# Kernel tuning notes

Hardware: AMD Instinct MI355X
Metric: run time of the kernel (lower is better)

The kernel has to match this reference:

```python
import jax, jax.numpy as jnp
import numpy as np
import math

EMBED_DIM = 512
NUM_CLASSES = 100000
BATCH = 512
MARGIN = 0.5
SCALE = 64.0
EASY_MARGIN = False
COS_M = math.cos(MARGIN)
SIN_M = math.sin(MARGIN)
TH = math.cos(math.pi - MARGIN)
MM = math.sin(math.pi - MARGIN) * MARGIN


def setup_inputs() -> dict:
    key = jax.random.key(0)
    k1, k2, k3 = jax.random.split(key, 3)
    inp = jax.random.normal(k1, (BATCH, EMBED_DIM), dtype=jnp.float32)
    # xavier-uniform init for weight [num_classes, embedding_dim]
    limit = math.sqrt(6.0 / (NUM_CLASSES + EMBED_DIM))
    weight = jax.random.uniform(k2, (NUM_CLASSES, EMBED_DIM), dtype=jnp.float32,
                                minval=-limit, maxval=limit)
    target = jax.random.randint(k3, (BATCH,), 0, NUM_CLASSES, dtype=jnp.int64)
    return {"input": inp, "weight": weight, "target": target}


def _l2_normalize(x, axis, eps=1e-12):
    # matches F.normalize(p=2): x / max(||x||, eps)
    n = jnp.sqrt(jnp.sum(x * x, axis=axis, keepdims=True))
    return x / jnp.maximum(n, eps)


def reference(input, weight, target):
    x = _l2_normalize(input, axis=1)                      # [B, D]
    w = _l2_normalize(weight, axis=1)                     # [C, D]
    cosine = jnp.einsum('bd,cd->bc', x, w)                # [B, C]
    # margin only affects the target logit; compute it per-row (same math as
    # the full-matrix where + one_hot blend in the original).
    cos_t = jnp.take_along_axis(cosine, target[:, None].astype(jnp.int32), axis=1)[:, 0]  # [B]
    sin_t = jnp.sqrt(jnp.clip(1.0 - cos_t * cos_t, 0.0, None))
    phi_t = cos_t * COS_M - sin_t * SIN_M
    if EASY_MARGIN:
        phi_t = jnp.where(cos_t > 0, phi_t, cos_t)
    else:
        phi_t = jnp.where(cos_t > TH, phi_t, cos_t - MM)
    # cross-entropy with scaled logits: logsumexp over modified logits - target logit
    # modified logits differ from `cosine*SCALE` only at the target column.
    rows = jnp.arange(cosine.shape[0])
    logits = cosine.at[rows, target.astype(jnp.int32)].set(phi_t) * SCALE  # [B, C]
    lse = jax.scipy.special.logsumexp(logits, axis=1)     # [B]
    loss = jnp.mean(lse - SCALE * phi_t)
    return loss
```

## Files before the change

### kernel.cpp

```cpp
#include <hip/hip_runtime.h>
#include <math.h>


#define NB 512
#define ND 512
#define NC 100000
#define BK 32
#define NCHUNK 16
#define CT 64
#define NTILE 1563
#define REP 64
#define FSCALE 64.0f
#define C_COS_M 0.8775825618903728f
#define C_SIN_M 0.479425538604203f
#define C_TH  (-0.8775825618903728f)
#define C_MM  0.2397127693021015f

#define SWZA(b) ((b) ^ (((b) >> 3) & 48))
#define SWZW(b) ((b) ^ (((b) >> 3) & 112))

typedef __bf16 bf16x8 __attribute__((ext_vector_type(8)));
typedef __bf16 bf16x4 __attribute__((ext_vector_type(4)));
typedef float  f32x4  __attribute__((ext_vector_type(4)));
typedef __attribute__((address_space(1))) unsigned int GU;
typedef __attribute__((address_space(3))) unsigned int LU;

__global__ void pack_x_kernel(const float* __restrict__ x, __bf16* __restrict__ xp) {
  const int b = blockIdx.x;
  const int t = threadIdx.x;
  float4 v = reinterpret_cast<const float4*>(x + (size_t)b * ND)[t];
  float ss = v.x*v.x + v.y*v.y + v.z*v.z + v.w*v.w;
  #pragma unroll
  for (int m = 1; m < 64; m <<= 1) ss += __shfl_xor(ss, m);
  __shared__ float sred[2];
  if ((t & 63) == 0) sred[t >> 6] = ss;
  __syncthreads();
  const float rn = rsqrtf(fmaxf(sred[0] + sred[1], 1e-24f));
  bf16x4 o;
  o[0] = (__bf16)(v.x * rn); o[1] = (__bf16)(v.y * rn);
  o[2] = (__bf16)(v.z * rn); o[3] = (__bf16)(v.w * rn);
  const int k = 4 * t;
  const int chunk = k >> 5;
  const int lb = b * 64 + (k & 31) * 2;
  char* dst = (char*)xp + (size_t)chunk * (NB * BK * 2) + SWZA(lb);
  *reinterpret_cast<bf16x4*>(dst) = o;
}

__global__ void prep_w_kernel(const float* __restrict__ w, __bf16* __restrict__ wp) {
  const int row  = blockIdx.x * 4 + (threadIdx.x >> 6);
  const int lane = threadIdx.x & 63;
  if (row >= NTILE * CT) return;
  const int srow = min(row, NC - 1);
  const float4* src = reinterpret_cast<const float4*>(w + (size_t)srow * ND);
  float4 v0 = src[lane * 2];
  float4 v1 = src[lane * 2 + 1];
  float ss = v0.x*v0.x + v0.y*v0.y + v0.z*v0.z + v0.w*v0.w
           + v1.x*v1.x + v1.y*v1.y + v1.z*v1.z + v1.w*v1.w;
  #pragma unroll
  for (int m = 1; m < 64; m <<= 1) ss += __shfl_xor(ss, m);
  float rn = rsqrtf(fmaxf(ss, 1e-24f));
  if (row >= NC) rn = 0.f;
  const int tile = row >> 6;
  const int r64  = row & 63;
  char* base = (char*)wp + (size_t)tile * (NCHUNK * 4096);
  #pragma unroll
  for (int j = 0; j < 2; ++j) {
    const float4 v = j ? v1 : v0;
    bf16x4 o;
    o[0] = (__bf16)(v.x * rn); o[1] = (__bf16)(v.y * rn);
    o[2] = (__bf16)(v.z * rn); o[3] = (__bf16)(v.w * rn);
    const int k  = lane * 8 + j * 4;
    const int lb = r64 * 64 + (k & 31) * 2;
    *reinterpret_cast<bf16x4*>(base + (k >> 5) * 4096 + SWZA(lb)) = o;
  }
}

__global__ void cosphi_kernel(const float* __restrict__ x, const float* __restrict__ w,
                              const int* __restrict__ tgt,
                              float* __restrict__ cos_t, float* __restrict__ phi_t) {
  const int b = blockIdx.x;
  const int lane = threadIdx.x;
  const int t = tgt[b];
  const float4* xr = reinterpret_cast<const float4*>(x + (size_t)b * ND);
  const float4* wr = reinterpret_cast<const float4*>(w + (size_t)t * ND);
  float dp = 0.f, xs = 0.f, ws = 0.f;
  #pragma unroll
  for (int j = 0; j < 2; ++j) {
    float4 xv = xr[lane * 2 + j];
    float4 wv = wr[lane * 2 + j];
    dp += xv.x*wv.x + xv.y*wv.y + xv.z*wv.z + xv.w*wv.w;
    xs += xv.x*xv.x + xv.y*xv.y + xv.z*xv.z + xv.w*xv.w;
    ws += wv.x*wv.x + wv.y*wv.y + wv.z*wv.z + wv.w*wv.w;
  }
  #pragma unroll
  for (int m = 1; m < 64; m <<= 1) {
    dp += __shfl_xor(dp, m);
    xs += __shfl_xor(xs, m);
    ws += __shfl_xor(ws, m);
  }
  if (lane == 0) {
    float c = dp * rsqrtf(fmaxf(xs, 1e-24f)) * rsqrtf(fmaxf(ws, 1e-24f));
    c = fminf(fmaxf(c, -1.f), 1.f);
    float s = sqrtf(fmaxf(1.f - c * c, 0.f));
    float phi = c * C_COS_M - s * C_SIN_M;
    phi = (c > C_TH) ? phi : (c - C_MM);
    cos_t[b] = c;
    phi_t[b] = phi;
  }
}

__global__ __launch_bounds__(512, 4) void gemm_lse_kernel(
    const __bf16* __restrict__ xp, const __bf16* __restrict__ wp,
    float* __restrict__ gsum) {
  __shared__ __align__(16) char As[2 * NB * BK * 2];
  __shared__ __align__(16) char Ws[2 * CT * BK * 2];

  const int tid  = threadIdx.x;
  const int wv   = tid >> 6;
  const int lane = tid & 63;
  const int bc   = blockIdx.x * CT;

  const char* ag = (const char*)xp + wv * 1024 + lane * 16;
  const char* wg = (const char*)wp + (size_t)blockIdx.x * (NCHUNK * 4096)
                   + wv * 1024 + lane * 16;

  {
    char* la = As + wv * 1024;
    #pragma unroll
    for (int j = 0; j < 4; ++j)
      __builtin_amdgcn_global_load_lds((const GU*)(ag + j * 8192),
                                       (LU*)(la + j * 8192), 16, 0, 0);
    if (wv < 4)
      __builtin_amdgcn_global_load_lds((const GU*)wg, (LU*)(Ws + wv * 1024),
                                       16, 0, 0);
  }

  const int m_w  = wv * 64;
  const int ra   = lane & 15;
  const int quad = lane >> 4;
  int aoff[4], boff[4];
  #pragma unroll
  for (int rt = 0; rt < 4; ++rt)
    aoff[rt] = SWZA((m_w + rt * 16 + ra) * 64 + quad * 16);
  #pragma unroll
  for (int ct = 0; ct < 4; ++ct)
    boff[ct] = SWZA((ct * 16 + ra) * 64 + quad * 16);

  f32x4 acc[4][4] = {};

  __syncthreads();

  for (int c = 0; c < NCHUNK; ++c) {
    const int cur = c & 1;
    if (c + 1 < NCHUNK) {
      const char* a1 = ag + (size_t)(c + 1) * (NB * BK * 2);
      char* la = As + (cur ^ 1) * (NB * BK * 2) + wv * 1024;
      #pragma unroll
      for (int j = 0; j < 4; ++j)
        __builtin_amdgcn_global_load_lds((const GU*)(a1 + j * 8192),
                                         (LU*)(la + j * 8192), 16, 0, 0);
      if (wv < 4)
        __builtin_amdgcn_global_load_lds((const GU*)(wg + (size_t)(c + 1) * 4096),
                                         (LU*)(Ws + (cur ^ 1) * 4096 + wv * 1024),
                                         16, 0, 0);
    }

    const char* asb = As + cur * (NB * BK * 2);
    const char* wsb = Ws + cur * 4096;
    bf16x8 af[4], bfr[4];
    #pragma unroll
    for (int rt = 0; rt < 4; ++rt)
      af[rt] = *reinterpret_cast<const bf16x8*>(asb + aoff[rt]);
    #pragma unroll
    for (int ct = 0; ct < 4; ++ct)
      bfr[ct] = *reinterpret_cast<const bf16x8*>(wsb + boff[ct]);
    #pragma unroll
    for (int rt = 0; rt < 4; ++rt)
      #pragma unroll
      for (int ct = 0; ct < 4; ++ct)
        acc[rt][ct] = __builtin_amdgcn_mfma_f32_16x16x32_bf16(af[rt], bfr[ct],
                                                              acc[rt][ct], 0, 0, 0);
    __syncthreads();
  }

  int vmask[4];
  #pragma unroll
  for (int ct = 0; ct < 4; ++ct)
    vmask[ct] = (bc + ct * 16 + ra) < NC;
  float* gs = gsum + (size_t)(blockIdx.x & (REP - 1)) * NB;
  #pragma unroll
  for (int rt = 0; rt < 4; ++rt) {
    #pragma unroll
    for (int rg = 0; rg < 4; ++rg) {
      float es = 0.f;
      #pragma unroll
      for (int ct = 0; ct < 4; ++ct) {
        float e = __expf(fmaf(FSCALE, acc[rt][ct][rg], -FSCALE));
        es += vmask[ct] ? e : 0.f;
      }
      es += __shfl_xor(es, 1);
      es += __shfl_xor(es, 2);
      es += __shfl_xor(es, 4);
      es += __shfl_xor(es, 8);
      if (ra == 0) {
        atomicAdd(&gs[m_w + rt * 16 + quad * 4 + rg], es);
      }
    }
  }
}

__global__ __launch_bounds__(512, 4) void gemm_lse_fb(
    const __bf16* __restrict__ xp, const float* __restrict__ w,
    float* __restrict__ gsum) {
  __shared__ __align__(16) char As[2 * NB * BK * 2];
  __shared__ __align__(16) char Ws[2 * CT * BK * 4];
  const int tid  = threadIdx.x;
  const int wv   = tid >> 6;
  const int lane = tid & 63;
  const int bc   = blockIdx.x * CT;
  const int p_w  = wv * 1024 + lane * 16;
  const int lbw  = SWZW(p_w);
  const int wrow = min(bc + (lbw >> 7), NC - 1);
  const char* wg = (const char*)w + (size_t)wrow * (ND * 4) + (lbw & 127);
  const char* ag = (const char*)xp + wv * 1024 + lane * 16;
  {
    char* la = As + wv * 1024;
    #pragma unroll
    for (int j = 0; j < 4; ++j)
      __builtin_amdgcn_global_load_lds((const GU*)(ag + j * 8192),
                                       (LU*)(la + j * 8192), 16, 0, 0);
    __builtin_amdgcn_global_load_lds((const GU*)wg, (LU*)(Ws + wv * 1024), 16, 0, 0);
  }
  const int m_w = wv * 64;
  const int ra = lane & 15;
  const int quad = lane >> 4;
  int aoff[4], woff[4];
  #pragma unroll
  for (int rt = 0; rt < 4; ++rt)
    aoff[rt] = SWZA((m_w + rt * 16 + ra) * 64 + quad * 16);
  #pragma unroll
  for (int ct = 0; ct < 4; ++ct)
    woff[ct] = SWZW((ct * 16 + ra) * 128 + quad * 32);
  f32x4 acc[4][4] = {};
  float wsq[4] = {0.f, 0.f, 0.f, 0.f};
  __syncthreads();
  for (int c = 0; c < NCHUNK; ++c) {
    const int cur = c & 1;
    if (c + 1 < NCHUNK) {
      const char* a1 = ag + (size_t)(c + 1) * (NB * BK * 2);
      char* la = As + (cur ^ 1) * (NB * BK * 2) + wv * 1024;
      #pragma unroll
      for (int j = 0; j < 4; ++j)
        __builtin_amdgcn_global_load_lds((const GU*)(a1 + j * 8192),
                                         (LU*)(la + j * 8192), 16, 0, 0);
      __builtin_amdgcn_global_load_lds((const GU*)(wg + (size_t)(c + 1) * 128),
                                       (LU*)(Ws + (cur ^ 1) * 8192 + wv * 1024),
                                       16, 0, 0);
    }
    const char* asb = As + cur * (NB * BK * 2);
    const char* wsb = Ws + cur * 8192;
    bf16x8 af[4];
    #pragma unroll
    for (int rt = 0; rt < 4; ++rt)
      af[rt] = *reinterpret_cast<const bf16x8*>(asb + aoff[rt]);
    #pragma unroll
    for (int ct = 0; ct < 4; ++ct) {
      float4 w0 = *reinterpret_cast<const float4*>(wsb + woff[ct]);
      float4 w1 = *reinterpret_cast<const float4*>(wsb + woff[ct] + 16);
      wsq[ct] += w0.x*w0.x + w0.y*w0.y + w0.z*w0.z + w0.w*w0.w
               + w1.x*w1.x + w1.y*w1.y + w1.z*w1.z + w1.w*w1.w;
      bf16x8 bfr;
      bfr[0] = (__bf16)w0.x; bfr[1] = (__bf16)w0.y;
      bfr[2] = (__bf16)w0.z; bfr[3] = (__bf16)w0.w;
      bfr[4] = (__bf16)w1.x; bfr[5] = (__bf16)w1.y;
      bfr[6] = (__bf16)w1.z; bfr[7] = (__bf16)w1.w;
      #pragma unroll
      for (int rt = 0; rt < 4; ++rt)
        acc[rt][ct] = __builtin_amdgcn_mfma_f32_16x16x32_bf16(af[rt], bfr,
                                                              acc[rt][ct], 0, 0, 0);
    }
    __syncthreads();
  }
  float rnw[4];
  int vmask[4];
  #pragma unroll
  for (int ct = 0; ct < 4; ++ct) {
    wsq[ct] += __shfl_xor(wsq[ct], 16);
    wsq[ct] += __shfl_xor(wsq[ct], 32);
    rnw[ct] = rsqrtf(fmaxf(wsq[ct], 1e-24f));
    vmask[ct] = (bc + ct * 16 + ra) < NC;
  }
  float* gs = gsum + (size_t)(blockIdx.x & (REP - 1)) * NB;
  #pragma unroll
  for (int rt = 0; rt < 4; ++rt) {
    #pragma unroll
    for (int rg = 0; rg < 4; ++rg) {
      float es = 0.f;
      #pragma unroll
      for (int ct = 0; ct < 4; ++ct) {
        float cosv = acc[rt][ct][rg] * rnw[ct];
        float e = __expf(fmaf(FSCALE, cosv, -FSCALE));
        es += vmask[ct] ? e : 0.f;
      }
      es += __shfl_xor(es, 1);
      es += __shfl_xor(es, 2);
      es += __shfl_xor(es, 4);
      es += __shfl_xor(es, 8);
      if (ra == 0) atomicAdd(&gs[m_w + rt * 16 + quad * 4 + rg], es);
    }
  }
}

__global__ void finalize_kernel(const float* __restrict__ gsum,
                                const float* __restrict__ cos_t,
                                const float* __restrict__ phi_t,
                                float* __restrict__ out) {
  const int b = threadIdx.x;
  float s = 0.f;
  #pragma unroll 8
  for (int r = 0; r < REP; ++r) s += gsum[r * NB + b];
  const float c = cos_t[b];
  const float p = phi_t[b];
  float corr = s - __expf(fmaf(FSCALE, c, -FSCALE))
                 + __expf(fmaf(FSCALE, p, -FSCALE));
  corr = fmaxf(corr, 1e-38f);
  float lb = FSCALE + logf(corr) - FSCALE * p;
  #pragma unroll
  for (int m = 1; m < 64; m <<= 1) lb += __shfl_xor(lb, m);
  __shared__ float pr[8];
  if ((b & 63) == 0) pr[b >> 6] = lb;
  __syncthreads();
  if (b == 0) {
    float tot = 0.f;
    #pragma unroll
    for (int j = 0; j < 8; ++j) tot += pr[j];
    out[0] = tot * (1.0f / NB);
  }
}

extern "C" void kernel_launch(void* const* d_in, const int* in_sizes, int n_in,
                              void* d_out, int out_size, void* d_ws, size_t ws_size,
                              hipStream_t stream) {
  const float* x  = (const float*)d_in[0];
  const float* w  = (const float*)d_in[1];
  const int* tgt  = (const int*)d_in[2];
  float* out      = (float*)d_out;

  __bf16* xp   = (__bf16*)d_ws;
  float* gsum  = (float*)((char*)d_ws + (size_t)NB * ND * 2);
  float* cos_t = gsum + (size_t)REP * NB;
  float* phi_t = cos_t + NB;
  const size_t WPOFF   = 1 << 20;
  const size_t WPBYTES = (size_t)NTILE * NCHUNK * 4096;
  __bf16* wp = (__bf16*)((char*)d_ws + WPOFF);

  hipMemsetAsync(gsum, 0, (size_t)REP * NB * sizeof(float), stream);
  pack_x_kernel<<<NB, 128, 0, stream>>>(x, xp);
  cosphi_kernel<<<NB, 64, 0, stream>>>(x, w, tgt, cos_t, phi_t);
  if (ws_size >= WPOFF + WPBYTES) {
    prep_w_kernel<<<(NTILE * CT) / 4, 256, 0, stream>>>(w, wp);
    gemm_lse_kernel<<<NTILE, 512, 0, stream>>>(xp, wp, gsum);
  } else {
    gemm_lse_fb<<<NTILE, 512, 0, stream>>>(xp, w, gsum);
  }
  finalize_kernel<<<1, 512, 0, stream>>>(gsum, cos_t, phi_t, out);
}
```

Baseline: 389.1 us.

## Retile GEMM to 256x128 blocks and rewrite weight prep with per-row 8-thread groups

The main GEMM now gives each block half the batch rows (256) and a 128-class tile, instead of all 512 rows and 64 classes. Shared memory per block shrinks and the occupancy hint rises from 4 to 6 blocks. Weight tiles are now 128 rows, and the prep kernel is rewritten so eight threads handle one row with a small shuffle reduction. This trades more re-reads of the small bf16 input matrix for higher occupancy and better per-block reuse of weights, and it changes the packed weight layout and the total work granularity.

```diff
diff --git a/kernel.cpp b/kernel.cpp
--- a/kernel.cpp
+++ b/kernel.cpp
@@ -9,6 +9,9 @@
 #define NCHUNK 16
 #define CT 64
 #define NTILE 1563
+#define CTW 128
+#define NTW 782
+#define WPT (NCHUNK * 8192)
 #define REP 64
 #define FSCALE 64.0f
 #define C_COS_M 0.8775825618903728f
@@ -46,32 +49,35 @@
   *reinterpret_cast<bf16x4*>(dst) = o;
 }
 
-__global__ void prep_w_kernel(const float* __restrict__ w, __bf16* __restrict__ wp) {
-  const int row  = blockIdx.x * 4 + (threadIdx.x >> 6);
-  const int lane = threadIdx.x & 63;
-  if (row >= NTILE * CT) return;
+__global__ __launch_bounds__(512) void prep_w_kernel(const float* __restrict__ w,
+                                                     __bf16* __restrict__ wp) {
+  const int t    = threadIdx.x;
+  const int row  = blockIdx.x * 64 + (t >> 3);
+  const int part = t & 7;
   const int srow = min(row, NC - 1);
   const float4* src = reinterpret_cast<const float4*>(w + (size_t)srow * ND);
-  float4 v0 = src[lane * 2];
-  float4 v1 = src[lane * 2 + 1];
-  float ss = v0.x*v0.x + v0.y*v0.y + v0.z*v0.z + v0.w*v0.w
-           + v1.x*v1.x + v1.y*v1.y + v1.z*v1.z + v1.w*v1.w;
-  #pragma unroll
-  for (int m = 1; m < 64; m <<= 1) ss += __shfl_xor(ss, m);
+  float4 v[16];
+  float ss = 0.f;
+  #pragma unroll
+  for (int j = 0; j < 16; ++j) {
+    v[j] = src[j * 8 + part];
+    ss += v[j].x*v[j].x + v[j].y*v[j].y + v[j].z*v[j].z + v[j].w*v[j].w;
+  }
+  ss += __shfl_xor(ss, 1);
+  ss += __shfl_xor(ss, 2);
+  ss += __shfl_xor(ss, 4);
   float rn = rsqrtf(fmaxf(ss, 1e-24f));
   if (row >= NC) rn = 0.f;
-  const int tile = row >> 6;
-  const int r64  = row & 63;
-  char* base = (char*)wp + (size_t)tile * (NCHUNK * 4096);
-  #pragma unroll
-  for (int j = 0; j < 2; ++j) {
-    const float4 v = j ? v1 : v0;
+  const int tile = row >> 7;
+  const int lrow = row & 127;
+  char* base = (char*)wp + (size_t)tile * WPT;
+  const int slot = SWZA(lrow * 64 + part * 8);
+  #pragma unroll
+  for (int j = 0; j < 16; ++j) {
     bf16x4 o;
-    o[0] = (__bf16)(v.x * rn); o[1] = (__bf16)(v.y * rn);
-    o[2] = (__bf16)(v.z * rn); o[3] = (__bf16)(v.w * rn);
-    const int k  = lane * 8 + j * 4;
-    const int lb = r64 * 64 + (k & 31) * 2;
-    *reinterpret_cast<bf16x4*>(base + (k >> 5) * 4096 + SWZA(lb)) = o;
+    o[0] = (__bf16)(v[j].x * rn); o[1] = (__bf16)(v[j].y * rn);
+    o[2] = (__bf16)(v[j].z * rn); o[3] = (__bf16)(v[j].w * rn);
+    *reinterpret_cast<bf16x4*>(base + j * 8192 + slot) = o;
   }
 }
 
@@ -109,42 +115,41 @@
   }
 }
 
-__global__ __launch_bounds__(512, 4) void gemm_lse_kernel(
+__global__ __launch_bounds__(512, 6) void gemm_lse_kernel(
     const __bf16* __restrict__ xp, const __bf16* __restrict__ wp,
     float* __restrict__ gsum) {
-  __shared__ __align__(16) char As[2 * NB * BK * 2];
-  __shared__ __align__(16) char Ws[2 * CT * BK * 2];
+  __shared__ __align__(16) char As[2 * 16384];
+  __shared__ __align__(16) char Ws[2 * 8192];
 
   const int tid  = threadIdx.x;
   const int wv   = tid >> 6;
   const int lane = tid & 63;
-  const int bc   = blockIdx.x * CT;
-
-  const char* ag = (const char*)xp + wv * 1024 + lane * 16;
-  const char* wg = (const char*)wp + (size_t)blockIdx.x * (NCHUNK * 4096)
-                   + wv * 1024 + lane * 16;
+  const int tile = blockIdx.x >> 1;
+  const int rh   = blockIdx.x & 1;
+  const int bc   = tile * CTW;
+
+  const char* ag = (const char*)xp + rh * 16384 + wv * 1024 + lane * 16;
+  const char* wg = (const char*)wp + (size_t)tile * WPT + wv * 1024 + lane * 16;
 
   {
+    __builtin_amdgcn_global_load_lds((const GU*)wg, (LU*)(Ws + wv * 1024), 16, 0, 0);
     char* la = As + wv * 1024;
-    #pragma unroll
-    for (int j = 0; j < 4; ++j)
-      __builtin_amdgcn_global_load_lds((const GU*)(ag + j * 8192),
-                                       (LU*)(la + j * 8192), 16, 0, 0);
-    if (wv < 4)
-      __builtin_amdgcn_global_load_lds((const GU*)wg, (LU*)(Ws + wv * 1024),
-                                       16, 0, 0);
-  }
-
-  const int m_w  = wv * 64;
+    __builtin_amdgcn_global_load_lds((const GU*)ag, (LU*)la, 16, 0, 0);
+    __builtin_amdgcn_global_load_lds((const GU*)(ag + 8192), (LU*)(la + 8192),
+                                     16, 0, 0);
+  }
+
+  const int wr   = wv >> 1;
+  const int wc   = wv & 1;
   const int ra   = lane & 15;
   const int quad = lane >> 4;
   int aoff[4], boff[4];
   #pragma unroll
   for (int rt = 0; rt < 4; ++rt)
-    aoff[rt] = SWZA((m_w + rt * 16 + ra) * 64 + quad * 16);
+    aoff[rt] = SWZA((wr * 64 + rt * 16 + ra) * 64 + quad * 16);
   #pragma unroll
   for (int ct = 0; ct < 4; ++ct)
-    boff[ct] = SWZA((ct * 16 + ra) * 64 + quad * 16);
+    boff[ct] = SWZA((wc * 64 + ct * 16 + ra) * 64 + quad * 16);
 
   f32x4 acc[4][4] = {};
 
@@ -153,20 +158,18 @@
   for (int c = 0; c < NCHUNK; ++c) {
     const int cur = c & 1;
     if (c + 1 < NCHUNK) {
-      const char* a1 = ag + (size_t)(c + 1) * (NB * BK * 2);
-      char* la = As + (cur ^ 1) * (NB * BK * 2) + wv * 1024;
-      #pragma unroll
-      for (int j = 0; j < 4; ++j)
-        __builtin_amdgcn_global_load_lds((const GU*)(a1 + j * 8192),
-                                         (LU*)(la + j * 8192), 16, 0, 0);
-      if (wv < 4)
-        __builtin_amdgcn_global_load_lds((const GU*)(wg + (size_t)(c + 1) * 4096),
-                                         (LU*)(Ws + (cur ^ 1) * 4096 + wv * 1024),
-                                         16, 0, 0);
-    }
-
-    const char* asb = As + cur * (NB * BK * 2);
-    const char* wsb = Ws + cur * 4096;
+      __builtin_amdgcn_global_load_lds(
+          (const GU*)(wg + (size_t)(c + 1) * 8192),
+          (LU*)(Ws + (cur ^ 1) * 8192 + wv * 1024), 16, 0, 0);
+      const char* a1 = ag + (size_t)(c + 1) * 32768;
+      char* la = As + (cur ^ 1) * 16384 + wv * 1024;
+      __builtin_amdgcn_global_load_lds((const GU*)a1, (LU*)la, 16, 0, 0);
+      __builtin_amdgcn_global_load_lds((const GU*)(a1 + 8192), (LU*)(la + 8192),
+                                       16, 0, 0);
+    }
+
+    const char* asb = As + cur * 16384;
+    const char* wsb = Ws + cur * 8192;
     bf16x8 af[4], bfr[4];
     #pragma unroll
     for (int rt = 0; rt < 4; ++rt)
@@ -186,8 +189,9 @@
   int vmask[4];
   #pragma unroll
   for (int ct = 0; ct < 4; ++ct)
-    vmask[ct] = (bc + ct * 16 + ra) < NC;
+    vmask[ct] = (bc + wc * 64 + ct * 16 + ra) < NC;
   float* gs = gsum + (size_t)(blockIdx.x & (REP - 1)) * NB;
+  const int rbase = rh * 256 + wr * 64;
   #pragma unroll
   for (int rt = 0; rt < 4; ++rt) {
     #pragma unroll
@@ -203,7 +207,7 @@
       es += __shfl_xor(es, 4);
       es += __shfl_xor(es, 8);
       if (ra == 0) {
-        atomicAdd(&gs[m_w + rt * 16 + quad * 4 + rg], es);
+        atomicAdd(&gs[rbase + rt * 16 + quad * 4 + rg], es);
       }
     }
   }
@@ -351,15 +355,15 @@
   float* cos_t = gsum + (size_t)REP * NB;
   float* phi_t = cos_t + NB;
   const size_t WPOFF   = 1 << 20;
-  const size_t WPBYTES = (size_t)NTILE * NCHUNK * 4096;
+  const size_t WPBYTES = (size_t)NTW * WPT;
   __bf16* wp = (__bf16*)((char*)d_ws + WPOFF);
 
   hipMemsetAsync(gsum, 0, (size_t)REP * NB * sizeof(float), stream);
   pack_x_kernel<<<NB, 128, 0, stream>>>(x, xp);
   cosphi_kernel<<<NB, 64, 0, stream>>>(x, w, tgt, cos_t, phi_t);
   if (ws_size >= WPOFF + WPBYTES) {
-    prep_w_kernel<<<(NTILE * CT) / 4, 256, 0, stream>>>(w, wp);
-    gemm_lse_kernel<<<NTILE, 512, 0, stream>>>(xp, wp, gsum);
+    prep_w_kernel<<<(NTW * CTW) / 64, 512, 0, stream>>>(w, wp);
+    gemm_lse_kernel<<<NTW * 2, 512, 0, stream>>>(xp, wp, gsum);
   } else {
     gemm_lse_fb<<<NTILE, 512, 0, stream>>>(xp, w, gsum);
   }
```

Measured after the change: 786.5 us. 102% more time.
